# Kernel optimization log

Hardware: AMD Instinct MI355X
Metric: run time of the kernel (lower is better)

The kernel has to match this reference:

```python
import jax, jax.numpy as jnp
import numpy as np

# --- config constants (from init_kwargs) ---
ALPHA = 0.05; SIGMA = 0.2; THETA = 0.3; A = 0.02; B_PAR = 0.1; RHO = 0.5
MULT = 2.0          # config.x_range_final[1]
GAMMA = 0.5         # power-utility exponent: u(x,r)=r*x^g/g, ux=r*x^(g-1)
N_STEPS = 100; T_FINAL = 1.0; DT = T_FINAL / N_STEPS
HID = 64; BATCH = 16384
PEN_SCALE = 100.0; LOWER = 1e-6


def _mlp(W1, b1, W2, b2, W3, b3, s):
    # tiny FeedForwardSubNet: 3 -> HID -> HID -> 1, tanh activations
    h = jnp.tanh(s @ W1 + b1)
    h = jnp.tanh(h @ W2 + b2)
    return h @ W3 + b3


def _penalise(v):
    # penalise_range(v, lower): quadratic hinge below `lower`
    return PEN_SCALE * jnp.square(jnp.maximum(LOWER - v, 0.0))


def setup_inputs() -> dict:
    key = jax.random.key(0)
    ks = jax.random.split(key, 16)
    dw = jax.random.normal(ks[0], (BATCH, 1, N_STEPS), dtype=jnp.float32) * float(np.sqrt(DT))
    X0 = jnp.ones((1,), jnp.float32)
    R0 = jnp.ones((1,), jnp.float32)
    def w(k, shape, fan):
        return jax.random.normal(k, shape, jnp.float32) / np.float32(np.sqrt(fan))
    inp = {"dw": dw, "X0": X0, "R0": R0,
           "pW1": w(ks[1], (3, HID), 3), "pb1": jnp.zeros((HID,), jnp.float32),
           "pW2": w(ks[2], (HID, HID), HID), "pb2": jnp.zeros((HID,), jnp.float32),
           "pW3": w(ks[3], (HID, 1), HID), "pb3": jnp.zeros((1,), jnp.float32),
           "qW1": w(ks[4], (3, HID), 3), "qb1": jnp.zeros((HID,), jnp.float32),
           "qW2": w(ks[5], (HID, HID), HID), "qb2": jnp.zeros((HID,), jnp.float32),
           "qW3": w(ks[6], (HID, 1), HID), "qb3": jnp.zeros((1,), jnp.float32)}
    return inp


def reference(dw, X0, R0, pW1, pb1, pW2, pb2, pW3, pb3, qW1, qb1, qW2, qb2, qW3, qb3):
    Bn = dw.shape[0]
    ones = jnp.ones((Bn, 1), dw.dtype)
    times = jnp.arange(N_STEPS + 1, dtype=dw.dtype) * DT   # [N+1]
    x0 = ones * X0
    R0v = ones * R0
    b_eff = float(np.sign(RHO)) * B_PAR

    # p_0 and dp_0 = d p_0 / d x (per-sample, rowwise independent net)
    def p_of_x(xx):
        st = jnp.concatenate([MULT * times[0] * ones, xx, R0v], 1)
        return _mlp(pW1, pb1, pW2, pb2, pW3, pb3, st)
    p0, p_vjp = jax.vjp(p_of_x, x0)
    (dp0,) = p_vjp(jnp.ones_like(p0))
    pi0 = _mlp(qW1, qb1, qW2, qb2, qW3, qb3,
               jnp.concatenate([MULT * times[0] * ones, x0, R0v], 1))

    dw_t = jnp.transpose(dw, (2, 0, 1))          # [N, B, 1]
    upd = jnp.arange(N_STEPS) < (N_STEPS - 1)    # pi not updated at last step

    def step(carry, inp):
        x, min_x, W, pi = carry
        dwi, t_next, u = inp
        x = x + x * ALPHA * DT + pi * SIGMA * THETA * DT + pi * SIGMA * dwi
        min_x = jnp.minimum(x, min_x)
        W = W + dwi
        Rv = R0v * jnp.exp((A - 0.5 * b_eff ** 2) * t_next + b_eff * W)
        p = p0 * jnp.exp(-(ALPHA + 0.5 * THETA ** 2) * t_next - THETA * W)
        st = jnp.concatenate([MULT * t_next * jnp.ones_like(x), x, Rv], 1)
        pi_new = _mlp(qW1, qb1, qW2, qb2, qW3, qb3, st)
        pi = jnp.where(u, pi_new, pi)
        return (x, min_x, W, pi), (x, Rv, pi, -p)

    (xf, min_x, Wf, pif), (xs, Rs, pis, dMs) = jax.lax.scan(
        step, (x0, x0, jnp.zeros_like(x0), pi0), (dw_t, times[1:], upd))

    # stacked process data, matching tf.concat-over-axis-0 ordering: [(N+1)*B, 1]
    x_all  = jnp.concatenate([x0[None], xs], 0).reshape(-1, 1)
    r_all  = jnp.concatenate([R0v[None], Rs], 0).reshape(-1, 1)
    pi_all = jnp.concatenate([pi0[None], pis], 0).reshape(-1, 1)
    dM_all = jnp.concatenate([(-p0)[None], dMs], 0).reshape(-1, 1)
    dM2_all = jnp.tile(-dp0, (N_STEPS + 1, 1))
    proc = jnp.concatenate([x_all, r_all, pi_all, dM_all, dM2_all], 1)  # [(N+1)*B, 5]

    # losses (non_concave = False branch)
    p_fin = -dMs[-1]
    R_fin = Rs[-1]
    xc = jnp.maximum(xf, LOWER)
    ux = R_fin * xc ** (GAMMA - 1.0)
    u_val = R_fin * xc ** GAMMA / GAMMA
    pen = _penalise(min_x)
    loss_p = jnp.mean(jnp.square(p_fin + ux) + pen)
    loss_pi = loss_p + jnp.mean(-u_val + pen)

    return jnp.concatenate([proc.reshape(-1), jnp.stack([loss_p, loss_pi])])
```

## Files before the change

### kernel.cpp

```cpp
#include <hip/hip_runtime.h>
#include <hip/hip_bf16.h>
#include <math.h>

#define NSTEP 100
#define BATCH 16384
#define MB 16
#define NBLK (BATCH/MB)
#define NT 64

#define C_ALPHA 0.05f
#define C_SIGMA 0.2f
#define C_THETA 0.3f
#define C_DT    0.01f
#define C_LOWER 1e-6f
#define C_PEN   100.0f
#define LOG2E   1.4426950408889634f
#define TSCALE  (2.0f * LOG2E)
#define CRT ( 0.015f * C_DT * LOG2E)
#define CRW ( 0.1f * LOG2E)
#define CPT (-0.095f * C_DT * LOG2E)
#define CPW (-0.3f * LOG2E)
#define XMUL (1.0f + C_ALPHA * C_DT)

typedef __attribute__((ext_vector_type(8))) short bf16x8;
typedef __attribute__((ext_vector_type(4))) float f32x4;

__device__ __forceinline__ float tanh_pre(float zs) {
    float e = __builtin_amdgcn_exp2f(zs);
    return 1.0f - 2.0f * __builtin_amdgcn_rcpf(e + 1.0f);
}
__device__ __forceinline__ unsigned f2bf_u(float f) {
    unsigned u = __float_as_uint(f);
    return (u + 0x7FFFu + ((u >> 16) & 1u)) >> 16;
}
__device__ __forceinline__ unsigned pack_bf16(float a, float b) {
    union { __hip_bfloat162 h; unsigned u; } cv;
    cv.h = __float22bfloat162_rn(make_float2(a, b));
    return cv.u;
}
__device__ __forceinline__ float dpp_row_sum16(float v) {
    int t;
    t = __builtin_amdgcn_update_dpp(0, __float_as_int(v), 0x128, 0xF, 0xF, true);
    v += __int_as_float(t);
    t = __builtin_amdgcn_update_dpp(0, __float_as_int(v), 0x124, 0xF, 0xF, true);
    v += __int_as_float(t);
    t = __builtin_amdgcn_update_dpp(0, __float_as_int(v), 0x122, 0xF, 0xF, true);
    v += __int_as_float(t);
    t = __builtin_amdgcn_update_dpp(0, __float_as_int(v), 0x121, 0xF, 0xF, true);
    v += __int_as_float(t);
    return v;
}

__global__ __launch_bounds__(NT, 1) void fused_kernel(
        const float* __restrict__ dw, const float* __restrict__ X0,
        const float* __restrict__ R0,
        const float* __restrict__ pW1, const float* __restrict__ pb1,
        const float* __restrict__ pW2, const float* __restrict__ pb2,
        const float* __restrict__ pW3, const float* __restrict__ pb3,
        const float* __restrict__ qW1, const float* __restrict__ qb1,
        const float* __restrict__ qW2, const float* __restrict__ qb2,
        const float* __restrict__ qW3, const float* __restrict__ qb3,
        float* __restrict__ ws, float* __restrict__ out) {
    __shared__ __align__(16) unsigned short sW2T[64 * 72];
    __shared__ __align__(16) float sdw[MB * NSTEP];
    __shared__ __align__(16) float sR[NSTEP * MB];
    __shared__ float sPf[MB];

    const int lane = threadIdx.x;
    const int b0 = blockIdx.x * MB;
    const int l15 = lane & 15, quad = lane >> 4;

    {
        const float4* g = (const float4*)(dw + (size_t)b0 * NSTEP);
        float4* s = (float4*)sdw;
        #pragma unroll
        for (int u = lane; u < MB * NSTEP / 4; u += NT) s[u] = g[u];
    }
    #pragma unroll 8
    for (int t = 0; t < 64; t++)
        sW2T[lane * 72 + t] = (unsigned short)f2bf_u(qW2[t * 64 + lane] * TSCALE);
    __syncthreads();

    const float X0v = X0[0], R0s = R0[0];
    const float b3 = qb3[0];

    float p0, dp0;
    {
        float pre = fmaf(pW1[64 + lane], X0v, fmaf(pW1[128 + lane], R0s, pb1[lane]));
        float h1 = tanh_pre(TSCALE * pre);
        float d1 = (1.0f - h1 * h1) * pW1[64 + lane];
        float a0 = pb2[lane], a1 = 0.f, a2 = 0.f, a3 = 0.f;
        float e0 = 0.f, e1 = 0.f, e2 = 0.f, e3 = 0.f;
        for (int i2 = 0; i2 < 64; i2 += 4) {
            float w0 = pW2[(i2 + 0) * 64 + lane];
            float w1 = pW2[(i2 + 1) * 64 + lane];
            float w2 = pW2[(i2 + 2) * 64 + lane];
            float w3 = pW2[(i2 + 3) * 64 + lane];
            a0 = fmaf(__shfl(h1, i2 + 0), w0, a0); e0 = fmaf(__shfl(d1, i2 + 0), w0, e0);
            a1 = fmaf(__shfl(h1, i2 + 1), w1, a1); e1 = fmaf(__shfl(d1, i2 + 1), w1, e1);
            a2 = fmaf(__shfl(h1, i2 + 2), w2, a2); e2 = fmaf(__shfl(d1, i2 + 2), w2, e2);
            a3 = fmaf(__shfl(h1, i2 + 3), w3, a3); e3 = fmaf(__shfl(d1, i2 + 3), w3, e3);
        }
        float pre2 = (a0 + a1) + (a2 + a3);
        float dpre2 = (e0 + e1) + (e2 + e3);
        float h2 = tanh_pre(TSCALE * pre2);
        float d2 = (1.0f - h2 * h2) * dpre2;
        float c1 = h2 * pW3[lane], c2 = d2 * pW3[lane];
        #pragma unroll
        for (int o = 1; o < 64; o <<= 1) {
            c1 += __shfl_xor(c1, o);
            c2 += __shfl_xor(c2, o);
        }
        p0 = c1 + pb3[0]; dp0 = c2;
    }

    {
        const int ps = lane >> 2;
        const int pc = lane & 3;
        float loc = 0.0f;
        #pragma unroll 5
        for (int j = pc * 25; j < pc * 25 + 25; j++) loc += sdw[ps * NSTEP + j];
        float o0 = __shfl(loc, ps * 4 + 0);
        float o1 = __shfl(loc, ps * 4 + 1);
        float o2 = __shfl(loc, ps * 4 + 2);
        float W = 0.0f;
        if (pc > 0) W += o0;
        if (pc > 1) W += o1;
        if (pc > 2) W += o2;
        #pragma unroll 5
        for (int t = pc * 25 + 1; t <= pc * 25 + 25; t++) {
            W += sdw[ps * NSTEP + (t - 1)];
            float ft = (float)t;
            float R = R0s * __builtin_amdgcn_exp2f(fmaf(CRW, W, CRT * ft));
            float pm = p0 * __builtin_amdgcn_exp2f(fmaf(CPW, W, CPT * ft));
            sR[(t - 1) * MB + ps] = R;
            size_t base = ((size_t)t * BATCH + b0 + ps) * 5;
            out[base + 1] = R; out[base + 3] = -pm; out[base + 4] = -dp0;
            if (t == NSTEP) sPf[ps] = pm;
        }
        if (lane < MB) {
            size_t base = (size_t)(b0 + lane) * 5;
            out[base] = X0v; out[base + 1] = R0s;
            out[base + 3] = -p0; out[base + 4] = -dp0;
        }
    }
    __syncthreads();

    bf16x8 Bf[4][2];
    #pragma unroll
    for (int nt = 0; nt < 4; nt++) {
        const unsigned short* r = &sW2T[(nt * 16 + l15) * 72 + quad * 8];
        Bf[nt][0] = *(const bf16x8*)r;
        Bf[nt][1] = *(const bf16x8*)(r + 32);
    }
    float tco[16], w1xs[16], w1rs[16], zc[16];
    #pragma unroll
    for (int idx = 0; idx < 16; idx++) {
        int k = (idx < 8) ? (quad * 8 + idx) : (32 + quad * 8 + (idx - 8));
        tco[idx]  = qW1[k] * (2.0f * C_DT * TSCALE);
        w1xs[idx] = qW1[64 + k] * TSCALE;
        w1rs[idx] = qW1[128 + k] * TSCALE;
        zc[idx]   = qb1[k] * TSCALE;
    }
    float b2v[4], w3v[4];
    #pragma unroll
    for (int nt = 0; nt < 4; nt++) {
        b2v[nt] = qb2[nt * 16 + l15] * TSCALE;
        w3v[nt] = qW3[nt * 16 + l15];
    }
    const int bperm_idx = (((l15 >> 2) * 16) + (l15 & 3)) * 4;

    auto l23 = [&](const bf16x8& A0, const bf16x8& A1) -> float {
        f32x4 acc0 = {b2v[0], b2v[0], b2v[0], b2v[0]};
        f32x4 acc1 = {b2v[1], b2v[1], b2v[1], b2v[1]};
        f32x4 acc2 = {b2v[2], b2v[2], b2v[2], b2v[2]};
        f32x4 acc3 = {b2v[3], b2v[3], b2v[3], b2v[3]};
        acc0 = __builtin_amdgcn_mfma_f32_16x16x32_bf16(A0, Bf[0][0], acc0, 0, 0, 0);
        acc1 = __builtin_amdgcn_mfma_f32_16x16x32_bf16(A0, Bf[1][0], acc1, 0, 0, 0);
        acc2 = __builtin_amdgcn_mfma_f32_16x16x32_bf16(A0, Bf[2][0], acc2, 0, 0, 0);
        acc3 = __builtin_amdgcn_mfma_f32_16x16x32_bf16(A0, Bf[3][0], acc3, 0, 0, 0);
        acc0 = __builtin_amdgcn_mfma_f32_16x16x32_bf16(A1, Bf[0][1], acc0, 0, 0, 0);
        acc1 = __builtin_amdgcn_mfma_f32_16x16x32_bf16(A1, Bf[1][1], acc1, 0, 0, 0);
        acc2 = __builtin_amdgcn_mfma_f32_16x16x32_bf16(A1, Bf[2][1], acc2, 0, 0, 0);
        acc3 = __builtin_amdgcn_mfma_f32_16x16x32_bf16(A1, Bf[3][1], acc3, 0, 0, 0);
        float th[16];
        #pragma unroll
        for (int r = 0; r < 4; r++) {
            th[r]      = tanh_pre(acc0[r]);
            th[4 + r]  = tanh_pre(acc1[r]);
            th[8 + r]  = tanh_pre(acc2[r]);
            th[12 + r] = tanh_pre(acc3[r]);
        }
        f32x4 part;
        #pragma unroll
        for (int r = 0; r < 4; r++) {
            float s = th[r] * w3v[0];
            s = fmaf(th[4 + r],  w3v[1], s);
            s = fmaf(th[8 + r],  w3v[2], s);
            s = fmaf(th[12 + r], w3v[3], s);
            part[r] = dpp_row_sum16(s);
        }
        float sLo = (lane & 1) ? part[1] : part[0];
        float sHi = (lane & 1) ? part[3] : part[2];
        float sel = (lane & 2) ? sHi : sLo;
        int g = __builtin_amdgcn_ds_bpermute(bperm_idx, __float_as_int(sel));
        return __int_as_float(g) + b3;
    };

    float pi;
    {
        union { bf16x8 v; unsigned u[4]; } A0, A1;
        float z[16];
        #pragma unroll
        for (int idx = 0; idx < 16; idx++)
            z[idx] = fmaf(w1rs[idx], R0s, fmaf(w1xs[idx], X0v, zc[idx]));
        float th[16];
        #pragma unroll
        for (int idx = 0; idx < 16; idx++) th[idx] = tanh_pre(z[idx]);
        #pragma unroll
        for (int p = 0; p < 4; p++) {
            A0.u[p] = pack_bf16(th[2 * p], th[2 * p + 1]);
            A1.u[p] = pack_bf16(th[8 + 2 * p], th[9 + 2 * p]);
        }
        pi = l23(A0.v, A1.v);
    }
    if (quad == 0) out[(size_t)(b0 + l15) * 5 + 2] = pi;

    float x = X0v, minx = X0v;
    float dw_cur = sdw[l15 * NSTEP];
    float R_cur = sR[l15];
    float* po = out + ((size_t)BATCH + b0 + l15) * 5;

    #pragma unroll 1
    for (int i = 0; i < NSTEP - 1; i++) {
        float dw_nx = sdw[l15 * NSTEP + i + 1];
        float R_nx  = sR[(i + 1) * MB + l15];
        float rz[16];
        #pragma unroll
        for (int idx = 0; idx < 16; idx++) {
            zc[idx] += tco[idx];
            rz[idx] = fmaf(w1rs[idx], R_cur, zc[idx]);
        }
        float xa = x * XMUL;
        float cdw = fmaf(C_SIGMA, dw_cur, C_SIGMA * C_THETA * C_DT);
        x = fmaf(pi, cdw, xa);
        minx = fminf(minx, x);
        if (quad == 0) po[0] = x;
        float z[16];
        #pragma unroll
        for (int idx = 0; idx < 16; idx++) z[idx] = fmaf(w1xs[idx], x, rz[idx]);
        float th[16];
        #pragma unroll
        for (int idx = 0; idx < 16; idx++) th[idx] = tanh_pre(z[idx]);
        union { bf16x8 v; unsigned u[4]; } A0, A1;
        #pragma unroll
        for (int p = 0; p < 4; p++) {
            A0.u[p] = pack_bf16(th[2 * p], th[2 * p + 1]);
            A1.u[p] = pack_bf16(th[8 + 2 * p], th[9 + 2 * p]);
        }
        float pin = l23(A0.v, A1.v);
        if (quad == 0) po[2] = pin;
        pi = pin;
        dw_cur = dw_nx; R_cur = R_nx;
        po += (size_t)BATCH * 5;
    }

    {
        float xa = x * XMUL;
        float cdw = fmaf(C_SIGMA, dw_cur, C_SIGMA * C_THETA * C_DT);
        x = fmaf(pi, cdw, xa);
        minx = fminf(minx, x);
        float Rf = R_cur;
        float pf = sPf[l15];
        if (quad == 0) { po[0] = x; po[2] = pi; }
        float xc = fmaxf(x, C_LOWER);
        float ux = Rf * rsqrtf(xc);
        float uval = 2.0f * Rf * sqrtf(xc);
        float d = fmaxf(C_LOWER - minx, 0.0f);
        float pen = C_PEN * d * d;
        float t1 = pf + ux;
        float v1 = dpp_row_sum16(t1 * t1 + pen);
        float v2 = dpp_row_sum16(-uval + pen);
        if (lane == 0) {
            atomicAdd(&ws[3], v1);
            atomicAdd(&ws[4], v2);
            __threadfence();
            int old = atomicAdd((int*)(ws + 5), 1);
            if (old == NBLK - 1) {
                float lp = atomicAdd(&ws[3], 0.0f) * (1.0f / (float)BATCH);
                float lq = atomicAdd(&ws[4], 0.0f) * (1.0f / (float)BATCH);
                out[(size_t)(NSTEP + 1) * BATCH * 5] = lp;
                out[(size_t)(NSTEP + 1) * BATCH * 5 + 1] = lp + lq;
            }
        }
    }
}

extern "C" void kernel_launch(void* const* d_in, const int* in_sizes, int n_in,
                              void* d_out, int out_size, void* d_ws, size_t ws_size,
                              hipStream_t stream) {
    const float* dw  = (const float*)d_in[0];
    const float* X0  = (const float*)d_in[1];
    const float* R0  = (const float*)d_in[2];
    const float* pW1 = (const float*)d_in[3];
    const float* pb1 = (const float*)d_in[4];
    const float* pW2 = (const float*)d_in[5];
    const float* pb2 = (const float*)d_in[6];
    const float* pW3 = (const float*)d_in[7];
    const float* pb3 = (const float*)d_in[8];
    const float* qW1 = (const float*)d_in[9];
    const float* qb1 = (const float*)d_in[10];
    const float* qW2 = (const float*)d_in[11];
    const float* qb2 = (const float*)d_in[12];
    const float* qW3 = (const float*)d_in[13];
    const float* qb3 = (const float*)d_in[14];
    float* out = (float*)d_out;
    float* ws  = (float*)d_ws;

    hipMemsetAsync(d_ws, 0, 64, stream);
    fused_kernel<<<NBLK, NT, 0, stream>>>(dw, X0, R0, pW1, pb1, pW2, pb2, pW3, pb3,
                                          qW1, qb1, qW2, qb2, qW3, qb3, ws, out);
}
```

Before: 217.3 us.

## Shrink samples per block to four and restructure prologue and output writes

Cuts samples per wave from 16 to 4, launching four times as many blocks so more independent latency-bound recurrences run in parallel per SIMD. The 16-row MFMA tile is now filled with replicated samples, so most matrix and tanh work per wave is redundant. W2 is packed to bf16 straight from global memory into registers instead of through an LDS transpose. The R/p outputs are written once per step together with x and pi instead of in a prologue pass, and the final ds_bpermute is dropped.

```diff
diff --git a/kernel.cpp b/kernel.cpp
--- a/kernel.cpp
+++ b/kernel.cpp
@@ -4,7 +4,7 @@
 
 #define NSTEP 100
 #define BATCH 16384
-#define MB 16
+#define MB 4
 #define NBLK (BATCH/MB)
 #define NT 64
 
@@ -29,10 +29,6 @@
     float e = __builtin_amdgcn_exp2f(zs);
     return 1.0f - 2.0f * __builtin_amdgcn_rcpf(e + 1.0f);
 }
-__device__ __forceinline__ unsigned f2bf_u(float f) {
-    unsigned u = __float_as_uint(f);
-    return (u + 0x7FFFu + ((u >> 16) & 1u)) >> 16;
-}
 __device__ __forceinline__ unsigned pack_bf16(float a, float b) {
     union { __hip_bfloat162 h; unsigned u; } cv;
     cv.h = __float22bfloat162_rn(make_float2(a, b));
@@ -51,7 +47,7 @@
     return v;
 }
 
-__global__ __launch_bounds__(NT, 1) void fused_kernel(
+__global__ __launch_bounds__(NT, 4) void fused_kernel(
         const float* __restrict__ dw, const float* __restrict__ X0,
         const float* __restrict__ R0,
         const float* __restrict__ pW1, const float* __restrict__ pb1,
@@ -61,28 +57,55 @@
         const float* __restrict__ qW2, const float* __restrict__ qb2,
         const float* __restrict__ qW3, const float* __restrict__ qb3,
         float* __restrict__ ws, float* __restrict__ out) {
-    __shared__ __align__(16) unsigned short sW2T[64 * 72];
     __shared__ __align__(16) float sdw[MB * NSTEP];
     __shared__ __align__(16) float sR[NSTEP * MB];
-    __shared__ float sPf[MB];
+    __shared__ __align__(16) float sPm[NSTEP * MB];
 
     const int lane = threadIdx.x;
     const int b0 = blockIdx.x * MB;
     const int l15 = lane & 15, quad = lane >> 4;
+    const int sl = l15 & 3;
 
     {
         const float4* g = (const float4*)(dw + (size_t)b0 * NSTEP);
         float4* s = (float4*)sdw;
-        #pragma unroll
         for (int u = lane; u < MB * NSTEP / 4; u += NT) s[u] = g[u];
     }
-    #pragma unroll 8
-    for (int t = 0; t < 64; t++)
-        sW2T[lane * 72 + t] = (unsigned short)f2bf_u(qW2[t * 64 + lane] * TSCALE);
-    __syncthreads();
-
     const float X0v = X0[0], R0s = R0[0];
     const float b3 = qb3[0];
+
+    bf16x8 Bf[4][2];
+    #pragma unroll
+    for (int nt = 0; nt < 4; nt++) {
+        const int col = nt * 16 + l15;
+        #pragma unroll
+        for (int ks = 0; ks < 2; ks++) {
+            float wb[8];
+            #pragma unroll
+            for (int j = 0; j < 8; j++)
+                wb[j] = qW2[(ks * 32 + quad * 8 + j) * 64 + col];
+            union { bf16x8 v; unsigned u[4]; } B;
+            #pragma unroll
+            for (int p = 0; p < 4; p++)
+                B.u[p] = pack_bf16(wb[2 * p] * TSCALE, wb[2 * p + 1] * TSCALE);
+            Bf[nt][ks] = B.v;
+        }
+    }
+    float tco[16], w1xs[16], w1rs[16], zc[16];
+    #pragma unroll
+    for (int idx = 0; idx < 16; idx++) {
+        int k = (idx < 8) ? (quad * 8 + idx) : (32 + quad * 8 + (idx - 8));
+        tco[idx]  = qW1[k] * (2.0f * C_DT * TSCALE);
+        w1xs[idx] = qW1[64 + k] * TSCALE;
+        w1rs[idx] = qW1[128 + k] * TSCALE;
+        zc[idx]   = qb1[k] * TSCALE;
+    }
+    float b2v[4], w3v[4];
+    #pragma unroll
+    for (int nt = 0; nt < 4; nt++) {
+        b2v[nt] = qb2[nt * 16 + l15] * TSCALE;
+        w3v[nt] = qW3[nt * 16 + l15];
+    }
 
     float p0, dp0;
     {
@@ -114,11 +137,10 @@
         p0 = c1 + pb3[0]; dp0 = c2;
     }
 
-    {
+    if (lane < 16) {
         const int ps = lane >> 2;
         const int pc = lane & 3;
         float loc = 0.0f;
-        #pragma unroll 5
         for (int j = pc * 25; j < pc * 25 + 25; j++) loc += sdw[ps * NSTEP + j];
         float o0 = __shfl(loc, ps * 4 + 0);
         float o1 = __shfl(loc, ps * 4 + 1);
@@ -127,48 +149,16 @@
         if (pc > 0) W += o0;
         if (pc > 1) W += o1;
         if (pc > 2) W += o2;
-        #pragma unroll 5
         for (int t = pc * 25 + 1; t <= pc * 25 + 25; t++) {
             W += sdw[ps * NSTEP + (t - 1)];
             float ft = (float)t;
-            float R = R0s * __builtin_amdgcn_exp2f(fmaf(CRW, W, CRT * ft));
-            float pm = p0 * __builtin_amdgcn_exp2f(fmaf(CPW, W, CPT * ft));
+            float R  = R0s * __builtin_amdgcn_exp2f(fmaf(CRW, W, CRT * ft));
+            float pm = p0  * __builtin_amdgcn_exp2f(fmaf(CPW, W, CPT * ft));
             sR[(t - 1) * MB + ps] = R;
-            size_t base = ((size_t)t * BATCH + b0 + ps) * 5;
-            out[base + 1] = R; out[base + 3] = -pm; out[base + 4] = -dp0;
-            if (t == NSTEP) sPf[ps] = pm;
-        }
-        if (lane < MB) {
-            size_t base = (size_t)(b0 + lane) * 5;
-            out[base] = X0v; out[base + 1] = R0s;
-            out[base + 3] = -p0; out[base + 4] = -dp0;
-        }
-    }
-    __syncthreads();
-
-    bf16x8 Bf[4][2];
-    #pragma unroll
-    for (int nt = 0; nt < 4; nt++) {
-        const unsigned short* r = &sW2T[(nt * 16 + l15) * 72 + quad * 8];
-        Bf[nt][0] = *(const bf16x8*)r;
-        Bf[nt][1] = *(const bf16x8*)(r + 32);
-    }
-    float tco[16], w1xs[16], w1rs[16], zc[16];
-    #pragma unroll
-    for (int idx = 0; idx < 16; idx++) {
-        int k = (idx < 8) ? (quad * 8 + idx) : (32 + quad * 8 + (idx - 8));
-        tco[idx]  = qW1[k] * (2.0f * C_DT * TSCALE);
-        w1xs[idx] = qW1[64 + k] * TSCALE;
-        w1rs[idx] = qW1[128 + k] * TSCALE;
-        zc[idx]   = qb1[k] * TSCALE;
-    }
-    float b2v[4], w3v[4];
-    #pragma unroll
-    for (int nt = 0; nt < 4; nt++) {
-        b2v[nt] = qb2[nt * 16 + l15] * TSCALE;
-        w3v[nt] = qW3[nt * 16 + l15];
-    }
-    const int bperm_idx = (((l15 >> 2) * 16) + (l15 & 3)) * 4;
+            sPm[(t - 1) * MB + ps] = pm;
+        }
+    } else {
+    }
 
     auto l23 = [&](const bf16x8& A0, const bf16x8& A1) -> float {
         f32x4 acc0 = {b2v[0], b2v[0], b2v[0], b2v[0]};
@@ -200,23 +190,20 @@
             s = fmaf(th[12 + r], w3v[3], s);
             part[r] = dpp_row_sum16(s);
         }
-        float sLo = (lane & 1) ? part[1] : part[0];
-        float sHi = (lane & 1) ? part[3] : part[2];
-        float sel = (lane & 2) ? sHi : sLo;
-        int g = __builtin_amdgcn_ds_bpermute(bperm_idx, __float_as_int(sel));
-        return __int_as_float(g) + b3;
+        float sLo = (l15 & 1) ? part[1] : part[0];
+        float sHi = (l15 & 1) ? part[3] : part[2];
+        return ((l15 & 2) ? sHi : sLo) + b3;
     };
 
     float pi;
     {
-        union { bf16x8 v; unsigned u[4]; } A0, A1;
-        float z[16];
+        float z[16], th[16];
         #pragma unroll
         for (int idx = 0; idx < 16; idx++)
             z[idx] = fmaf(w1rs[idx], R0s, fmaf(w1xs[idx], X0v, zc[idx]));
-        float th[16];
         #pragma unroll
         for (int idx = 0; idx < 16; idx++) th[idx] = tanh_pre(z[idx]);
+        union { bf16x8 v; unsigned u[4]; } A0, A1;
         #pragma unroll
         for (int p = 0; p < 4; p++) {
             A0.u[p] = pack_bf16(th[2 * p], th[2 * p + 1]);
@@ -224,17 +211,22 @@
         }
         pi = l23(A0.v, A1.v);
     }
-    if (quad == 0) out[(size_t)(b0 + l15) * 5 + 2] = pi;
+    if (quad == 0 && l15 < MB) {
+        float* po = out + (size_t)(b0 + sl) * 5;
+        po[0] = X0v; po[1] = R0s; po[2] = pi; po[3] = -p0; po[4] = -dp0;
+    }
 
     float x = X0v, minx = X0v;
-    float dw_cur = sdw[l15 * NSTEP];
-    float R_cur = sR[l15];
-    float* po = out + ((size_t)BATCH + b0 + l15) * 5;
+    float dw_cur = sdw[sl * NSTEP];
+    float R_cur  = sR[sl];
+    float Pm_cur = sPm[sl];
+    float* po = out + ((size_t)BATCH + b0 + sl) * 5;
 
     #pragma unroll 1
     for (int i = 0; i < NSTEP - 1; i++) {
-        float dw_nx = sdw[l15 * NSTEP + i + 1];
-        float R_nx  = sR[(i + 1) * MB + l15];
+        float dw_nx = sdw[sl * NSTEP + i + 1];
+        float R_nx  = sR[(i + 1) * MB + sl];
+        float Pm_nx = sPm[(i + 1) * MB + sl];
         float rz[16];
         #pragma unroll
         for (int idx = 0; idx < 16; idx++) {
@@ -245,11 +237,9 @@
         float cdw = fmaf(C_SIGMA, dw_cur, C_SIGMA * C_THETA * C_DT);
         x = fmaf(pi, cdw, xa);
         minx = fminf(minx, x);
-        if (quad == 0) po[0] = x;
-        float z[16];
+        float z[16], th[16];
         #pragma unroll
         for (int idx = 0; idx < 16; idx++) z[idx] = fmaf(w1xs[idx], x, rz[idx]);
-        float th[16];
         #pragma unroll
         for (int idx = 0; idx < 16; idx++) th[idx] = tanh_pre(z[idx]);
         union { bf16x8 v; unsigned u[4]; } A0, A1;
@@ -259,9 +249,11 @@
             A1.u[p] = pack_bf16(th[8 + 2 * p], th[9 + 2 * p]);
         }
         float pin = l23(A0.v, A1.v);
-        if (quad == 0) po[2] = pin;
+        if (quad == 0 && l15 < MB) {
+            po[0] = x; po[1] = R_cur; po[2] = pin; po[3] = -Pm_cur; po[4] = -dp0;
+        }
         pi = pin;
-        dw_cur = dw_nx; R_cur = R_nx;
+        dw_cur = dw_nx; R_cur = R_nx; Pm_cur = Pm_nx;
         po += (size_t)BATCH * 5;
     }
 
@@ -271,16 +263,21 @@
         x = fmaf(pi, cdw, xa);
         minx = fminf(minx, x);
         float Rf = R_cur;
-        float pf = sPf[l15];
-        if (quad == 0) { po[0] = x; po[2] = pi; }
+        float pf = Pm_cur;
+        if (quad == 0 && l15 < MB) {
+            po[0] = x; po[1] = Rf; po[2] = pi; po[3] = -pf; po[4] = -dp0;
+        }
         float xc = fmaxf(x, C_LOWER);
         float ux = Rf * rsqrtf(xc);
         float uval = 2.0f * Rf * sqrtf(xc);
         float d = fmaxf(C_LOWER - minx, 0.0f);
         float pen = C_PEN * d * d;
         float t1 = pf + ux;
-        float v1 = dpp_row_sum16(t1 * t1 + pen);
-        float v2 = dpp_row_sum16(-uval + pen);
+        bool active = (quad == 0 && l15 < MB);
+        float v1 = active ? (t1 * t1 + pen) : 0.0f;
+        float v2 = active ? (-uval + pen) : 0.0f;
+        v1 = dpp_row_sum16(v1);
+        v2 = dpp_row_sum16(v2);
         if (lane == 0) {
             atomicAdd(&ws[3], v1);
             atomicAdd(&ws[4], v2);
```

Result: slower. 510.2 us (+134.7%).
